# Kernel tuning notes

Hardware: AMD Instinct MI355X
Metric: run time of the kernel (lower is better)

The kernel has to match this reference:

```python
import jax, jax.numpy as jnp
import numpy as np

N_HEADS = 16


def setup_inputs() -> dict:
    key = jax.random.key(0)
    ks = jax.random.split(key, 10)
    B, M, N, C, D = 2, 2048, 2048, 1024, 1024
    s = 0.02
    return {
        "kv": jax.random.normal(ks[0], (B, M, C), jnp.float32),
        "q": jax.random.normal(ks[1], (B, N, D), jnp.float32),
        "Wk": jax.random.normal(ks[2], (C, D), jnp.float32) * s,
        "bk": jnp.zeros((D,), jnp.float32),
        "Wq": jax.random.normal(ks[3], (D, D), jnp.float32) * s,
        "bq": jnp.zeros((D,), jnp.float32),
        "Wv": jax.random.normal(ks[4], (C, D), jnp.float32) * s,
        "bv": jnp.zeros((D,), jnp.float32),
        "Wp": jax.random.normal(ks[5], (D, D), jnp.float32) * s,
        "bp": jnp.zeros((D,), jnp.float32),
    }


def reference(kv, q, Wk, bk, Wq, bq, Wv, bv, Wp, bp):
    B, M, C = kv.shape
    B2, N, D = q.shape
    H = N_HEADS
    hd = D // H
    # projections (weights stored as [in, out]; torch Linear is x @ W.T + b with W [out,in])
    k = (kv @ Wk + bk).reshape(B, M, H, hd).transpose(0, 2, 1, 3)  # [B,H,M,hd]
    qh = (q @ Wq + bq).reshape(B, N, H, hd).transpose(0, 2, 1, 3)  # [B,H,N,hd]
    v = (kv @ Wv + bv).reshape(B, M, H, hd).transpose(0, 2, 1, 3)  # [B,H,M,hd]
    scale = 1.0 / jnp.sqrt(jnp.asarray(hd, k.dtype))
    att = jnp.einsum("bhnd,bhmd->bhnm", qh, k) * scale
    att = jax.nn.softmax(att, axis=-1)
    y = jnp.einsum("bhnm,bhmd->bhnd", att, v)  # [B,H,N,hd]
    y = y.transpose(0, 2, 1, 3).reshape(B, N, D)
    return y @ Wp + bp
```

## Files before the change

kernel.cpp:

```cpp
#include <hip/hip_runtime.h>

#define DV 1024
#define HD 64

typedef short v4s __attribute__((ext_vector_type(4)));
typedef short v8s __attribute__((ext_vector_type(8)));
typedef float v4f __attribute__((ext_vector_type(4)));
typedef int   v2i __attribute__((ext_vector_type(2)));

__device__ __forceinline__ short f2bf(float x){
  unsigned u = __float_as_uint(x);
  u += 0x7FFFu + ((u >> 16) & 1u);
  return (short)(u >> 16);
}

__device__ __forceinline__ int swz(int lane){
  return (((lane & 7) ^ (lane >> 3)) << 3);
}

__global__ __launch_bounds__(256) void cvt2(const float* __restrict__ xa,
                                            const float* __restrict__ xb,
                                            short* __restrict__ ya,
                                            short* __restrict__ yb, int n){
  const float* x = blockIdx.y ? xb : xa;
  short* y = blockIdx.y ? yb : ya;
  int stride = gridDim.x * 256 * 4;
  for (int i = (blockIdx.x * 256 + threadIdx.x) * 4; i < n; i += stride){
    float4 v = *(const float4*)(x + i);
    v4s s; s.x = f2bf(v.x); s.y = f2bf(v.y); s.z = f2bf(v.z); s.w = f2bf(v.w);
    *(v4s*)(y + i) = s;
  }
}

__global__ __launch_bounds__(256) void tcvt4(
    const float* __restrict__ W0, const float* __restrict__ W1,
    const float* __restrict__ W2, const float* __restrict__ W3,
    short* __restrict__ T0, short* __restrict__ T1,
    short* __restrict__ T2, short* __restrict__ T3){
  const float* W; short* Wt;
  switch (blockIdx.z){
    case 0: W = W0; Wt = T0; break;
    case 1: W = W1; Wt = T1; break;
    case 2: W = W2; Wt = T2; break;
    default: W = W3; Wt = T3; break;
  }
  __shared__ short L[64 * 68];
  const int t = threadIdx.x;
  const int k0 = blockIdx.y * 64, n0 = blockIdx.x * 64;
  const int rr = t >> 4, cc = (t & 15) * 4;
  #pragma unroll
  for (int j = 0; j < 4; j++){
    int r = rr + j * 16;
    float4 v = *(const float4*)(W + (size_t)(k0 + r) * DV + n0 + cc);
    v4s s; s.x = f2bf(v.x); s.y = f2bf(v.y); s.z = f2bf(v.z); s.w = f2bf(v.w);
    *(v4s*)&L[r * 68 + cc] = s;
  }
  __syncthreads();
  #pragma unroll
  for (int j = 0; j < 4; j++){
    int n = rr + j * 16;
    v4s s;
    s.x = L[(cc + 0) * 68 + n];
    s.y = L[(cc + 1) * 68 + n];
    s.z = L[(cc + 2) * 68 + n];
    s.w = L[(cc + 3) * 68 + n];
    *(v4s*)(Wt + (size_t)(n0 + n) * DV + k0 + cc) = s;
  }
}

template<typename OUT_T>
__device__ __forceinline__ void gemm_tile(
    const short* __restrict__ A, const short* __restrict__ Bt,
    const float* __restrict__ bias, OUT_T* __restrict__ C,
    int M, int N, int K, float out_scale, int m0, int n0, bool bias_row)
{
  __shared__ short As[128 * 64];
  __shared__ short Bs[128 * 64];
  const int tid = threadIdx.x;
  const int wave = tid >> 6, lane = tid & 63;
  const int quad = lane >> 4, l15 = lane & 15;
  const int wr = (wave >> 1) * 64, wc = (wave & 1) * 64;
  const int srow = lane >> 3;
  const int sw = swz(lane);
  const v4f vzero = {0.f, 0.f, 0.f, 0.f};

  const short* pa[4]; const short* pb[4];
  #pragma unroll
  for (int ii = 0; ii < 4; ii++){
    int i = wave * 4 + ii;
    pa[ii] = A  + (size_t)(m0 + i * 8 + srow) * K + sw;
    pb[ii] = Bt + (size_t)(n0 + i * 8 + srow) * K + sw;
  }

  v8s ra[4], rb[4];
  #pragma unroll
  for (int ii = 0; ii < 4; ii++){
    ra[ii] = *(const v8s*)(pa[ii]);
    rb[ii] = *(const v8s*)(pb[ii]);
  }

  v4f acc[4][4];
  #pragma unroll
  for (int i = 0; i < 4; i++)
    #pragma unroll
    for (int j = 0; j < 4; j++)
      acc[i][j] = vzero;

  for (int kt = 0; kt < K; kt += 64){
    __syncthreads();
    #pragma unroll
    for (int ii = 0; ii < 4; ii++){
      int i = wave * 4 + ii;
      *(v8s*)&As[i * 512 + lane * 8] = ra[ii];
      *(v8s*)&Bs[i * 512 + lane * 8] = rb[ii];
    }
    __syncthreads();
    if (kt + 64 < K){
      #pragma unroll
      for (int ii = 0; ii < 4; ii++){
        ra[ii] = *(const v8s*)(pa[ii] + kt + 64);
        rb[ii] = *(const v8s*)(pb[ii] + kt + 64);
      }
    }
    #pragma unroll
    for (int ks = 0; ks < 2; ks++){
      v8s a[4], b[4];
      #pragma unroll
      for (int mt = 0; mt < 4; mt++)
        a[mt] = *(const v8s*)&As[(wr + mt * 16 + l15) * 64 + (((ks * 4 + quad) ^ (l15 & 7)) << 3)];
      #pragma unroll
      for (int nt = 0; nt < 4; nt++)
        b[nt] = *(const v8s*)&Bs[(wc + nt * 16 + l15) * 64 + (((ks * 4 + quad) ^ (l15 & 7)) << 3)];
      #pragma unroll
      for (int mt = 0; mt < 4; mt++)
        #pragma unroll
        for (int nt = 0; nt < 4; nt++)
          acc[mt][nt] = __builtin_amdgcn_mfma_f32_16x16x32_bf16(a[mt], b[nt], acc[mt][nt], 0, 0, 0);
    }
  }

  #pragma unroll
  for (int mt = 0; mt < 4; mt++){
    #pragma unroll
    for (int nt = 0; nt < 4; nt++){
      int row = m0 + wr + mt * 16 + quad * 4;
      int col = n0 + wc + nt * 16 + l15;
      float bcol = bias_row ? 0.0f : bias[col];
      #pragma unroll
      for (int r = 0; r < 4; r++){
        float bv = bias_row ? bias[row + r] : bcol;
        float v = (acc[mt][nt][r] + bv) * out_scale;
        if (sizeof(OUT_T) == 2)
          ((short*)C)[(size_t)(row + r) * N + col] = f2bf(v);
        else
          ((float*)C)[(size_t)(row + r) * N + col] = v;
      }
    }
  }
}

__global__ __launch_bounds__(256, 3) void proj3(
    const short* __restrict__ qb, const short* __restrict__ kvb,
    const short* __restrict__ Wqt, const short* __restrict__ Wkt,
    const short* __restrict__ Wvt,
    const float* __restrict__ bq, const float* __restrict__ bk,
    const float* __restrict__ bv,
    short* __restrict__ Qp, short* __restrict__ Kp, short* __restrict__ VT,
    float qscale)
{
  int bid = blockIdx.x;
  const short *A, *Bt; const float* bias; short* C;
  int M, N, m0, n0; float scale; bool brow;
  if (bid < 512){
    int z = bid >> 8, l = bid & 255;
    M = 4096; N = 1024; m0 = (l & 31) * 128; n0 = (l >> 5) * 128;
    A = z ? kvb : qb; Bt = z ? Wkt : Wqt; bias = z ? bk : bq;
    C = z ? Kp : Qp; scale = z ? 1.0f : qscale; brow = false;
  } else {
    int l = bid - 512;
    M = 1024; N = 4096; m0 = (l >> 5) * 128; n0 = (l & 31) * 128;
    A = Wvt; Bt = kvb; bias = bv; C = VT; scale = 1.0f; brow = true;
  }
  gemm_tile<short>(A, Bt, bias, C, M, N, 1024, scale, m0, n0, brow);
}

__global__ __launch_bounds__(256, 2) void gemm_f32(
    const short* __restrict__ A, const short* __restrict__ Bt,
    const float* __restrict__ bias, float* __restrict__ C)
{
  __shared__ short As[128 * 64];
  __shared__ short Bs[64 * 64];
  const int tid = threadIdx.x;
  const int wave = tid >> 6, lane = tid & 63;
  const int quad = lane >> 4, l15 = lane & 15;
  const int bid = blockIdx.x;
  const int m0 = (bid & 31) * 128, n0 = (bid >> 5) * 64;
  const int wr = (wave >> 1) * 64, wc = (wave & 1) * 32;
  const int srow = lane >> 3;
  const int sw = swz(lane);
  const int K = 1024;
  const v4f vzero = {0.f, 0.f, 0.f, 0.f};

  const short* pa[4]; const short* pb[2];
  #pragma unroll
  for (int ii = 0; ii < 4; ii++)
    pa[ii] = A + (size_t)(m0 + (wave * 4 + ii) * 8 + srow) * K + sw;
  #pragma unroll
  for (int ii = 0; ii < 2; ii++)
    pb[ii] = Bt + (size_t)(n0 + (wave * 2 + ii) * 8 + srow) * K + sw;

  v8s ra[4], rb[2];
  #pragma unroll
  for (int ii = 0; ii < 4; ii++) ra[ii] = *(const v8s*)(pa[ii]);
  #pragma unroll
  for (int ii = 0; ii < 2; ii++) rb[ii] = *(const v8s*)(pb[ii]);

  v4f acc[4][2];
  #pragma unroll
  for (int i = 0; i < 4; i++){ acc[i][0] = vzero; acc[i][1] = vzero; }

  for (int kt = 0; kt < K; kt += 64){
    __syncthreads();
    #pragma unroll
    for (int ii = 0; ii < 4; ii++)
      *(v8s*)&As[(wave * 4 + ii) * 512 + lane * 8] = ra[ii];
    #pragma unroll
    for (int ii = 0; ii < 2; ii++)
      *(v8s*)&Bs[(wave * 2 + ii) * 512 + lane * 8] = rb[ii];
    __syncthreads();
    if (kt + 64 < K){
      #pragma unroll
      for (int ii = 0; ii < 4; ii++) ra[ii] = *(const v8s*)(pa[ii] + kt + 64);
      #pragma unroll
      for (int ii = 0; ii < 2; ii++) rb[ii] = *(const v8s*)(pb[ii] + kt + 64);
    }
    #pragma unroll
    for (int ks = 0; ks < 2; ks++){
      v8s a[4], b[2];
      #pragma unroll
      for (int mt = 0; mt < 4; mt++)
        a[mt] = *(const v8s*)&As[(wr + mt * 16 + l15) * 64 + (((ks * 4 + quad) ^ (l15 & 7)) << 3)];
      #pragma unroll
      for (int nt = 0; nt < 2; nt++)
        b[nt] = *(const v8s*)&Bs[(wc + nt * 16 + l15) * 64 + (((ks * 4 + quad) ^ (l15 & 7)) << 3)];
      #pragma unroll
      for (int mt = 0; mt < 4; mt++)
        #pragma unroll
        for (int nt = 0; nt < 2; nt++)
          acc[mt][nt] = __builtin_amdgcn_mfma_f32_16x16x32_bf16(a[mt], b[nt], acc[mt][nt], 0, 0, 0);
    }
  }

  #pragma unroll
  for (int mt = 0; mt < 4; mt++){
    #pragma unroll
    for (int nt = 0; nt < 2; nt++){
      int row = m0 + wr + mt * 16 + quad * 4;
      int col = n0 + wc + nt * 16 + l15;
      float bcol = bias[col];
      #pragma unroll
      for (int r = 0; r < 4; r++)
        C[(size_t)(row + r) * 1024 + col] = acc[mt][nt][r] + bcol;
    }
  }
}

__global__ __launch_bounds__(256, 4) void attn(
    const short* __restrict__ Qp, const short* __restrict__ Kp,
    const short* __restrict__ Vt, short* __restrict__ Y)
{
  __shared__ short Ks[2][64 * 64];
  __shared__ short Vs[2][64 * 72];
  const int tid = threadIdx.x;
  const int wave = tid >> 6, lane = tid & 63;
  const int quad = lane >> 4, l15 = lane & 15;
  const int gid = blockIdx.x;
  const int qi = gid >> 5, bh = gid & 31;
  const int h = bh & 15, b = bh >> 4;
  const int n0 = qi * 64;
  const int srow = lane >> 3;
  const int c8 = (lane & 7) * 8;
  const int sw = swz(lane);
  const size_t rowbase = (size_t)b * 2048;
  const v4f vzero = {0.f, 0.f, 0.f, 0.f};

  v8s qf[2];
  {
    const short* qrow = Qp + (rowbase + n0 + wave * 16 + l15) * DV + h * HD + quad * 8;
    qf[0] = *(const v8s*)(qrow);
    qf[1] = *(const v8s*)(qrow + 32);
  }

  const short* pk[2]; const short* pv[2];
  #pragma unroll
  for (int ii = 0; ii < 2; ii++){
    int i = wave * 2 + ii;
    pk[ii] = Kp + (rowbase + i * 8 + srow) * DV + h * HD + sw;
    pv[ii] = Vt + (size_t)(h * HD + i * 8 + srow) * 4096 + rowbase + c8;
  }
  v8s rk[2][2], rv[2][2];
  #pragma unroll
  for (int tt = 0; tt < 2; tt++)
    #pragma unroll
    for (int ii = 0; ii < 2; ii++){
      rk[tt][ii] = *(const v8s*)(pk[ii] + (size_t)tt * 64 * DV);
      rv[tt][ii] = *(const v8s*)(pv[ii] + tt * 64);
    }

  v4f o[4];
  #pragma unroll
  for (int dt = 0; dt < 4; dt++) o[dt] = vzero;
  float lsum = 0.0f;

  for (int t = 0; t < 16; t++){
    __syncthreads();
    #pragma unroll
    for (int tt = 0; tt < 2; tt++)
      #pragma unroll
      for (int ii = 0; ii < 2; ii++){
        int i = wave * 2 + ii;
        *(v8s*)&Ks[tt][i * 512 + lane * 8] = rk[tt][ii];
        *(v8s*)&Vs[tt][(i * 8 + srow) * 72 + c8] = rv[tt][ii];
      }
    __syncthreads();
    if (t < 15){
      #pragma unroll
      for (int tt = 0; tt < 2; tt++)
        #pragma unroll
        for (int ii = 0; ii < 2; ii++){
          rk[tt][ii] = *(const v8s*)(pk[ii] + (size_t)(2 * t + 2 + tt) * 64 * DV);
          rv[tt][ii] = *(const v8s*)(pv[ii] + (2 * t + 2 + tt) * 64);
        }
    }

    #pragma unroll
    for (int tt = 0; tt < 2; tt++){
      v4f s[4];
      #pragma unroll
      for (int kvt = 0; kvt < 4; kvt++) s[kvt] = vzero;
      #pragma unroll
      for (int ks = 0; ks < 2; ks++){
        v8s a[4];
        #pragma unroll
        for (int kvt = 0; kvt < 4; kvt++)
          a[kvt] = *(const v8s*)&Ks[tt][(kvt * 16 + l15) * 64 + (((ks * 4 + quad) ^ (l15 & 7)) << 3)];
        #pragma unroll
        for (int kvt = 0; kvt < 4; kvt++)
          s[kvt] = __builtin_amdgcn_mfma_f32_16x16x32_bf16(a[kvt], qf[ks], s[kvt], 0, 0, 0);
      }

      v4s pf[4];
      #pragma unroll
      for (int kvt = 0; kvt < 4; kvt++){
        float p0 = __builtin_amdgcn_exp2f(s[kvt][0]);
        float p1 = __builtin_amdgcn_exp2f(s[kvt][1]);
        float p2 = __builtin_amdgcn_exp2f(s[kvt][2]);
        float p3 = __builtin_amdgcn_exp2f(s[kvt][3]);
        lsum += (p0 + p1) + (p2 + p3);
        unsigned u0 = __float_as_uint(p0) + 0x8000u;
        unsigned u1 = __float_as_uint(p1) + 0x8000u;
        unsigned u2 = __float_as_uint(p2) + 0x8000u;
        unsigned u3 = __float_as_uint(p3) + 0x8000u;
        v2i pi;
        pi.x = (int)__builtin_amdgcn_perm(u1, u0, 0x07060302u);
        pi.y = (int)__builtin_amdgcn_perm(u3, u2, 0x07060302u);
        pf[kvt] = __builtin_bit_cast(v4s, pi);
      }

      #pragma unroll
      for (int ks = 0; ks < 4; ks++){
        v4s a[4];
        #pragma unroll
        for (int dt = 0; dt < 4; dt++)
          a[dt] = *(const v4s*)&Vs[tt][(dt * 16 + l15) * 72 + ks * 16 + quad * 4];
        #pragma unroll
        for (int dt = 0; dt < 4; dt++)
          o[dt] = __builtin_amdgcn_mfma_f32_16x16x16bf16_1k(a[dt], pf[ks], o[dt], 0, 0, 0);
      }
    }
  }

  lsum += __shfl_xor(lsum, 16);
  lsum += __shfl_xor(lsum, 32);
  float inv = 1.0f / lsum;
  size_t row = rowbase + n0 + wave * 16 + l15;
  #pragma unroll
  for (int dt = 0; dt < 4; dt++){
    int col = h * HD + dt * 16 + quad * 4;
    unsigned p0 = (unsigned short)f2bf(o[dt][0] * inv) |
                  ((unsigned)(unsigned short)f2bf(o[dt][1] * inv) << 16);
    unsigned p1 = (unsigned short)f2bf(o[dt][2] * inv) |
                  ((unsigned)(unsigned short)f2bf(o[dt][3] * inv) << 16);
    *(unsigned*)(Y + row * DV + col)     = p0;
    *(unsigned*)(Y + row * DV + col + 2) = p1;
  }
}

extern "C" void kernel_launch(void* const* d_in, const int* in_sizes, int n_in,
                              void* d_out, int out_size, void* d_ws, size_t ws_size,
                              hipStream_t stream) {
  const float* kv = (const float*)d_in[0];
  const float* q  = (const float*)d_in[1];
  const float* Wk = (const float*)d_in[2];
  const float* bk = (const float*)d_in[3];
  const float* Wq = (const float*)d_in[4];
  const float* bq = (const float*)d_in[5];
  const float* Wv = (const float*)d_in[6];
  const float* bv = (const float*)d_in[7];
  const float* Wp = (const float*)d_in[8];
  const float* bp = (const float*)d_in[9];

  const size_t E  = 4194304;
  const size_t WE = 1048576;
  short* p   = (short*)d_ws;
  short* kvb = p; p += E;
  short* qb  = p; p += E;
  short* Wkt = p; p += WE;
  short* Wqt = p; p += WE;
  short* Wvt = p; p += WE;
  short* Wpt = p; p += WE;
  short* Kp  = p; p += E;
  short* Qp  = p; p += E;
  short* VT  = p; p += E;
  short* Yb  = p; p += E;

  cvt2<<<dim3(512, 2), 256, 0, stream>>>(kv, q, kvb, qb, (int)E);
  tcvt4<<<dim3(16, 16, 4), 256, 0, stream>>>(Wk, Wq, Wv, Wp, Wkt, Wqt, Wvt, Wpt);

  proj3<<<768, 256, 0, stream>>>(qb, kvb, Wqt, Wkt, Wvt, bq, bk, bv,
                                 Qp, Kp, VT, 0.18033688011f);

  attn<<<1024, 256, 0, stream>>>(Qp, Kp, VT, Yb);

  gemm_f32<<<512, 256, 0, stream>>>(Yb, Wpt, bp, (float*)d_out);
}
```

Baseline: 232.2 us.

## Double query rows per attention block to reuse K/V tiles

Each attention block now handles 128 query rows (32 per wave, two 16-row sub-tiles) instead of 64, so every K/V tile staged in shared memory feeds twice as many MFMAs. The loop stages one 64-row KV tile per iteration instead of two, and the V padding drops from 72 to 68. The grid is halved to 512 blocks and launch bounds lowered to 3, giving more registers per thread at the cost of fewer resident blocks and less parallelism across CUs.

```diff
diff --git a/kernel.cpp b/kernel.cpp
--- a/kernel.cpp
+++ b/kernel.cpp
@@ -265,30 +265,31 @@
   }
 }
 
-__global__ __launch_bounds__(256, 4) void attn(
+__global__ __launch_bounds__(256, 3) void attn(
     const short* __restrict__ Qp, const short* __restrict__ Kp,
     const short* __restrict__ Vt, short* __restrict__ Y)
 {
-  __shared__ short Ks[2][64 * 64];
-  __shared__ short Vs[2][64 * 72];
+  __shared__ short Ks[64 * 64];
+  __shared__ short Vs[64 * 68];
   const int tid = threadIdx.x;
   const int wave = tid >> 6, lane = tid & 63;
   const int quad = lane >> 4, l15 = lane & 15;
   const int gid = blockIdx.x;
   const int qi = gid >> 5, bh = gid & 31;
   const int h = bh & 15, b = bh >> 4;
-  const int n0 = qi * 64;
+  const int n0 = qi * 128;
   const int srow = lane >> 3;
   const int c8 = (lane & 7) * 8;
   const int sw = swz(lane);
   const size_t rowbase = (size_t)b * 2048;
   const v4f vzero = {0.f, 0.f, 0.f, 0.f};
 
-  v8s qf[2];
-  {
-    const short* qrow = Qp + (rowbase + n0 + wave * 16 + l15) * DV + h * HD + quad * 8;
-    qf[0] = *(const v8s*)(qrow);
-    qf[1] = *(const v8s*)(qrow + 32);
+  v8s qf[2][2];
+  #pragma unroll
+  for (int qt = 0; qt < 2; qt++){
+    const short* qrow = Qp + (rowbase + n0 + wave * 32 + qt * 16 + l15) * DV + h * HD + quad * 8;
+    qf[qt][0] = *(const v8s*)(qrow);
+    qf[qt][1] = *(const v8s*)(qrow + 32);
   }
 
   const short* pk[2]; const short* pv[2];
@@ -298,65 +299,60 @@
     pk[ii] = Kp + (rowbase + i * 8 + srow) * DV + h * HD + sw;
     pv[ii] = Vt + (size_t)(h * HD + i * 8 + srow) * 4096 + rowbase + c8;
   }
-  v8s rk[2][2], rv[2][2];
-  #pragma unroll
-  for (int tt = 0; tt < 2; tt++)
+  v8s rk[2], rv[2];
+  #pragma unroll
+  for (int ii = 0; ii < 2; ii++){ rk[ii] = *(const v8s*)(pk[ii]); rv[ii] = *(const v8s*)(pv[ii]); }
+
+  v4f o[4][2];
+  #pragma unroll
+  for (int dt = 0; dt < 4; dt++){ o[dt][0] = vzero; o[dt][1] = vzero; }
+  float lsum[2] = {0.0f, 0.0f};
+
+  for (int kt = 0; kt < 32; kt++){
+    __syncthreads();
     #pragma unroll
     for (int ii = 0; ii < 2; ii++){
-      rk[tt][ii] = *(const v8s*)(pk[ii] + (size_t)tt * 64 * DV);
-      rv[tt][ii] = *(const v8s*)(pv[ii] + tt * 64);
-    }
-
-  v4f o[4];
-  #pragma unroll
-  for (int dt = 0; dt < 4; dt++) o[dt] = vzero;
-  float lsum = 0.0f;
-
-  for (int t = 0; t < 16; t++){
-    __syncthreads();
-    #pragma unroll
-    for (int tt = 0; tt < 2; tt++)
+      int i = wave * 2 + ii;
+      *(v8s*)&Ks[i * 512 + lane * 8] = rk[ii];
+      *(v8s*)&Vs[(i * 8 + srow) * 68 + c8] = rv[ii];
+    }
+    __syncthreads();
+    if (kt < 31){
       #pragma unroll
       for (int ii = 0; ii < 2; ii++){
-        int i = wave * 2 + ii;
-        *(v8s*)&Ks[tt][i * 512 + lane * 8] = rk[tt][ii];
-        *(v8s*)&Vs[tt][(i * 8 + srow) * 72 + c8] = rv[tt][ii];
+        rk[ii] = *(const v8s*)(pk[ii] + (size_t)(kt + 1) * 64 * DV);
+        rv[ii] = *(const v8s*)(pv[ii] + (kt + 1) * 64);
       }
-    __syncthreads();
-    if (t < 15){
-      #pragma unroll
-      for (int tt = 0; tt < 2; tt++)
+    }
+
+    v4f s[2][4];
+    #pragma unroll
+    for (int qt = 0; qt < 2; qt++)
+      #pragma unroll
+      for (int kvt = 0; kvt < 4; kvt++) s[qt][kvt] = vzero;
+    #pragma unroll
+    for (int ks = 0; ks < 2; ks++){
+      v8s a[4];
+      #pragma unroll
+      for (int kvt = 0; kvt < 4; kvt++)
+        a[kvt] = *(const v8s*)&Ks[(kvt * 16 + l15) * 64 + (((ks * 4 + quad) ^ (l15 & 7)) << 3)];
+      #pragma unroll
+      for (int kvt = 0; kvt < 4; kvt++)
         #pragma unroll
-        for (int ii = 0; ii < 2; ii++){
-          rk[tt][ii] = *(const v8s*)(pk[ii] + (size_t)(2 * t + 2 + tt) * 64 * DV);
-          rv[tt][ii] = *(const v8s*)(pv[ii] + (2 * t + 2 + tt) * 64);
-        }
-    }
-
-    #pragma unroll
-    for (int tt = 0; tt < 2; tt++){
-      v4f s[4];
-      #pragma unroll
-      for (int kvt = 0; kvt < 4; kvt++) s[kvt] = vzero;
-      #pragma unroll
-      for (int ks = 0; ks < 2; ks++){
-        v8s a[4];
-        #pragma unroll
-        for (int kvt = 0; kvt < 4; kvt++)
-          a[kvt] = *(const v8s*)&Ks[tt][(kvt * 16 + l15) * 64 + (((ks * 4 + quad) ^ (l15 & 7)) << 3)];
-        #pragma unroll
-        for (int kvt = 0; kvt < 4; kvt++)
-          s[kvt] = __builtin_amdgcn_mfma_f32_16x16x32_bf16(a[kvt], qf[ks], s[kvt], 0, 0, 0);
-      }
-
-      v4s pf[4];
+        for (int qt = 0; qt < 2; qt++)
+          s[qt][kvt] = __builtin_amdgcn_mfma_f32_16x16x32_bf16(a[kvt], qf[qt][ks], s[qt][kvt], 0, 0, 0);
+    }
+
+    v4s pf[2][4];
+    #pragma unroll
+    for (int qt = 0; qt < 2; qt++)
       #pragma unroll
       for (int kvt = 0; kvt < 4; kvt++){
-        float p0 = __builtin_amdgcn_exp2f(s[kvt][0]);
-        float p1 = __builtin_amdgcn_exp2f(s[kvt][1]);
-        float p2 = __builtin_amdgcn_exp2f(s[kvt][2]);
-        float p3 = __builtin_amdgcn_exp2f(s[kvt][3]);
-        lsum += (p0 + p1) + (p2 + p3);
+        float p0 = __builtin_amdgcn_exp2f(s[qt][kvt][0]);
+        float p1 = __builtin_amdgcn_exp2f(s[qt][kvt][1]);
+        float p2 = __builtin_amdgcn_exp2f(s[qt][kvt][2]);
+        float p3 = __builtin_amdgcn_exp2f(s[qt][kvt][3]);
+        lsum[qt] += (p0 + p1) + (p2 + p3);
         unsigned u0 = __float_as_uint(p0) + 0x8000u;
         unsigned u1 = __float_as_uint(p1) + 0x8000u;
         unsigned u2 = __float_as_uint(p2) + 0x8000u;
@@ -364,35 +360,40 @@
         v2i pi;
         pi.x = (int)__builtin_amdgcn_perm(u1, u0, 0x07060302u);
         pi.y = (int)__builtin_amdgcn_perm(u3, u2, 0x07060302u);
-        pf[kvt] = __builtin_bit_cast(v4s, pi);
+        pf[qt][kvt] = __builtin_bit_cast(v4s, pi);
       }
 
-      #pragma unroll
-      for (int ks = 0; ks < 4; ks++){
-        v4s a[4];
+    #pragma unroll
+    for (int ks = 0; ks < 4; ks++){
+      v4s a[4];
+      #pragma unroll
+      for (int dt = 0; dt < 4; dt++)
+        a[dt] = *(const v4s*)&Vs[(dt * 16 + l15) * 68 + ks * 16 + quad * 4];
+      #pragma unroll
+      for (int dt = 0; dt < 4; dt++)
         #pragma unroll
-        for (int dt = 0; dt < 4; dt++)
-          a[dt] = *(const v4s*)&Vs[tt][(dt * 16 + l15) * 72 + ks * 16 + quad * 4];
-        #pragma unroll
-        for (int dt = 0; dt < 4; dt++)
-          o[dt] = __builtin_amdgcn_mfma_f32_16x16x16bf16_1k(a[dt], pf[ks], o[dt], 0, 0, 0);
-      }
-    }
-  }
-
-  lsum += __shfl_xor(lsum, 16);
-  lsum += __shfl_xor(lsum, 32);
-  float inv = 1.0f / lsum;
-  size_t row = rowbase + n0 + wave * 16 + l15;
-  #pragma unroll
-  for (int dt = 0; dt < 4; dt++){
-    int col = h * HD + dt * 16 + quad * 4;
-    unsigned p0 = (unsigned short)f2bf(o[dt][0] * inv) |
-                  ((unsigned)(unsigned short)f2bf(o[dt][1] * inv) << 16);
-    unsigned p1 = (unsigned short)f2bf(o[dt][2] * inv) |
-                  ((unsigned)(unsigned short)f2bf(o[dt][3] * inv) << 16);
-    *(unsigned*)(Y + row * DV + col)     = p0;
-    *(unsigned*)(Y + row * DV + col + 2) = p1;
+        for (int qt = 0; qt < 2; qt++)
+          o[dt][qt] = __builtin_amdgcn_mfma_f32_16x16x16bf16_1k(a[dt], pf[qt][ks], o[dt][qt], 0, 0, 0);
+    }
+  }
+
+  #pragma unroll
+  for (int qt = 0; qt < 2; qt++){
+    float ls = lsum[qt];
+    ls += __shfl_xor(ls, 16);
+    ls += __shfl_xor(ls, 32);
+    float inv = 1.0f / ls;
+    size_t row = rowbase + n0 + wave * 32 + qt * 16 + l15;
+    #pragma unroll
+    for (int dt = 0; dt < 4; dt++){
+      int col = h * HD + dt * 16 + quad * 4;
+      unsigned p0 = (unsigned short)f2bf(o[dt][qt][0] * inv) |
+                    ((unsigned)(unsigned short)f2bf(o[dt][qt][1] * inv) << 16);
+      unsigned p1 = (unsigned short)f2bf(o[dt][qt][2] * inv) |
+                    ((unsigned)(unsigned short)f2bf(o[dt][qt][3] * inv) << 16);
+      *(unsigned*)(Y + row * DV + col)     = p0;
+      *(unsigned*)(Y + row * DV + col + 2) = p1;
+    }
   }
 }
 
@@ -430,7 +431,7 @@
   proj3<<<768, 256, 0, stream>>>(qb, kvb, Wqt, Wkt, Wvt, bq, bk, bv,
                                  Qp, Kp, VT, 0.18033688011f);
 
-  attn<<<1024, 256, 0, stream>>>(Qp, Kp, VT, Yb);
+  attn<<<512, 256, 0, stream>>>(Qp, Kp, VT, Yb);
 
   gemm_f32<<<512, 256, 0, stream>>>(Yb, Wpt, bp, (float*)d_out);
 }
```

Result: faster. 204.8 us (-11.8%).
